# Performance work log

Hardware: AMD Instinct MI355X
Metric: run time of the kernel (lower is better)

## Reference

```python
import jax, jax.numpy as jnp
import numpy as np

B, H_IMG, W_IMG, DIM, HEADS, WS = 8, 56, 56, 768, 12, 14
SEQ = H_IMG * W_IMG
HEAD_DIM = DIM // HEADS
MLP_HID = 4 * DIM
SCALE = HEAD_DIM ** -0.5


def setup_inputs() -> dict:
    key = jax.random.key(0)
    ks = jax.random.split(key, 8)
    s = 0.02
    return {
        "x": jax.random.normal(ks[0], (B, SEQ, DIM), jnp.float32),
        "ln1_scale": jnp.ones((DIM,), jnp.float32),
        "ln1_bias": jnp.zeros((DIM,), jnp.float32),
        "qkv_w": jax.random.normal(ks[1], (DIM, 3 * DIM), jnp.float32) * s,
        "qkv_b": jnp.zeros((3 * DIM,), jnp.float32),
        "rel_pos_h": jax.random.normal(ks[2], (2 * WS - 1, HEAD_DIM), jnp.float32) * s,
        "rel_pos_w": jax.random.normal(ks[3], (2 * WS - 1, HEAD_DIM), jnp.float32) * s,
        "proj_w": jax.random.normal(ks[4], (DIM, DIM), jnp.float32) * s,
        "proj_b": jnp.zeros((DIM,), jnp.float32),
        "ln2_scale": jnp.ones((DIM,), jnp.float32),
        "ln2_bias": jnp.zeros((DIM,), jnp.float32),
        "fc1_w": jax.random.normal(ks[5], (DIM, MLP_HID), jnp.float32) * s,
        "fc1_b": jnp.zeros((MLP_HID,), jnp.float32),
        "fc2_w": jax.random.normal(ks[6], (MLP_HID, DIM), jnp.float32) * s,
        "fc2_b": jnp.zeros((DIM,), jnp.float32),
        "H": H_IMG,
        "W": W_IMG,
    }


def _layernorm(x, scale, bias, eps=1e-5):
    mu = x.mean(-1, keepdims=True)
    var = x.var(-1, keepdims=True)
    return (x - mu) / jnp.sqrt(var + eps) * scale + bias


def _window_attn(x, H, W, qkv_w, qkv_b, rel_pos_h, rel_pos_w, proj_w, proj_b):
    # x: (B, H*W, C); H, W divisible by WS so the torch pad branch is a no-op
    Bn, N, C = x.shape
    nh, nw = H // WS, W // WS
    # window_partition: (B, H, W, C) -> (B*nh*nw, WS*WS, C)
    xw = (x.reshape(Bn, nh, WS, nw, WS, C)
            .transpose(0, 1, 3, 2, 4, 5)
            .reshape(-1, WS * WS, C))
    Bw, Nw = xw.shape[0], WS * WS
    qkv = (xw @ qkv_w + qkv_b).reshape(Bw, Nw, 3, HEADS, HEAD_DIM).transpose(2, 0, 3, 1, 4)
    q = qkv[0] * SCALE  # scaled q also used for rel-pos terms (matches torch)
    k, v = qkv[1], qkv[2]
    attn = jnp.einsum('bhnd,bhmd->bhnm', q, k)  # (Bw, heads, Nw, Nw)
    # relative position bias (q_shape == k_shape == (WS, WS), ratios == 1)
    dist = jnp.arange(WS)[:, None] - jnp.arange(WS)[None, :] + (WS - 1)
    Rh = rel_pos_h[dist]  # (WS, WS, head_dim)
    Rw = rel_pos_w[dist]
    r_q = q.reshape(Bw, HEADS, WS, WS, HEAD_DIM)
    rel_h = jnp.einsum('byhwc,hkc->byhwk', r_q, Rh)
    rel_w = jnp.einsum('byhwc,wkc->byhwk', r_q, Rw)
    attn = (attn.reshape(Bw, HEADS, WS, WS, WS, WS)
            + rel_h[:, :, :, :, :, None]
            + rel_w[:, :, :, :, None, :]).reshape(Bw, HEADS, Nw, Nw)
    attn = jax.nn.softmax(attn, axis=-1)
    out = jnp.einsum('bhnm,bhmd->bhnd', attn, v).transpose(0, 2, 1, 3).reshape(Bw, Nw, C)
    out = out @ proj_w + proj_b
    # window_reverse: (Bw, WS*WS, C) -> (B, H*W, C)
    out = (out.reshape(Bn, nh, nw, WS, WS, C)
              .transpose(0, 1, 3, 2, 4, 5)
              .reshape(Bn, H * W, C))
    return out


def reference(x, ln1_scale, ln1_bias, qkv_w, qkv_b, rel_pos_h, rel_pos_w,
              proj_w, proj_b, ln2_scale, ln2_bias, fc1_w, fc1_b, fc2_w, fc2_b, H, W):
    a = _window_attn(_layernorm(x, ln1_scale, ln1_bias), H, W,
                     qkv_w, qkv_b, rel_pos_h, rel_pos_w, proj_w, proj_b)
    x = x + a
    h = _layernorm(x, ln2_scale, ln2_bias)
    h = jax.nn.gelu(h @ fc1_w + fc1_b, approximate=False)  # torch nn.GELU is exact erf
    x = x + (h @ fc2_w + fc2_b)
    return x
```

## Files before the change

### kernel.cpp

```cpp
#include <hip/hip_runtime.h>
#include <stdint.h>

typedef unsigned short u16;
typedef __bf16 bf16x8 __attribute__((ext_vector_type(8)));
typedef float f32x4 __attribute__((ext_vector_type(4)));
typedef unsigned uint32x4 __attribute__((ext_vector_type(4)));

#define DEVI __device__ __forceinline__

static constexpr int DIM = 768;
static constexpr int SEQL = 3136;
static constexpr int MROWS = 25088;
static constexpr int HEADS = 12;
static constexpr int HD = 64;
static constexpr int NW = 196;
static constexpr float QSCALE = 0.125f;
static constexpr int ATTN_SMEM = 72704;
static constexpr int GEMM_SMEM = 49152;

DEVI float b2f(u16 u) { union { unsigned i; float f; } v; v.i = ((unsigned)u) << 16; return v.f; }
DEVI u16 f2b(float f) { union { float f; unsigned u; } v; v.f = f; return (u16)((v.u + 0x7FFFu + ((v.u >> 16) & 1u)) >> 16); }
DEVI unsigned pack2(float a, float b) { return (unsigned)f2b(a) | ((unsigned)f2b(b) << 16); }
DEVI bf16x8 u4bf(uint4 u) { union { uint4 a; bf16x8 b; } c; c.a = u; return c.b; }

DEVI void gl_lds16(const void* g, void* l) {
  __builtin_amdgcn_global_load_lds((const __attribute__((address_space(1))) void*)g,
                                   (__attribute__((address_space(3))) void*)l, 16, 0, 0);
}

DEVI bf16x8 ldg_b8(const u16* p) {
  union { uint4 u; bf16x8 v; } r;
  const uint2* p2 = (const uint2*)p;
  uint2 lo = p2[0], hi = p2[1];
  r.u.x = lo.x; r.u.y = lo.y; r.u.z = hi.x; r.u.w = hi.y;
  return r.v;
}

__global__ __launch_bounds__(256) void pack_b(const float* __restrict__ in,
                                              u16* __restrict__ out, int K, int N) {
  int f8 = blockIdx.x * 256 + threadIdx.x;
  int l = f8 & 63;
  int rest = f8 >> 6;
  int s = rest & 1, nf = (rest >> 1) & 3, wn2 = (rest >> 3) & 1, kt = rest >> 4;
  int bn = blockIdx.y;
  int n = bn * 128 + wn2 * 64 + nf * 16 + (l & 15);
  int kb = kt * 64 + s * 32 + (l >> 4) * 8;
  size_t obase = (((size_t)bn * (K >> 6) + kt) * 2 + wn2) * 4096 + (nf * 2 + s) * 512 + (size_t)l * 8;
  #pragma unroll
  for (int e = 0; e < 8; ++e)
    out[obase + e] = f2b(in[(size_t)(kb + e) * N + n]);
}

__global__ __launch_bounds__(256) void cvt_rpb(const float* __restrict__ rph,
                                               const float* __restrict__ rpw,
                                               u16* __restrict__ rpb) {
  int i = blockIdx.x * 256 + threadIdx.x;
  int tbl = i >> 11, r = (i >> 6) & 31, c = i & 63;
  float v = (r < 27) ? (tbl ? rpw : rph)[r * 64 + c] : 0.f;
  rpb[i] = f2b(v);
}

template<bool REMAP>
__global__ __launch_bounds__(256) void ln_kernel(const float* __restrict__ xin,
                                                 const float* __restrict__ g,
                                                 const float* __restrict__ bb,
                                                 u16* __restrict__ outw) {
  __shared__ float red[8];
  const int r = blockIdx.x;
  const int tid = threadIdx.x;
  const float* xr = xin + (size_t)r * DIM;
  float v0 = xr[tid], v1 = xr[tid + 256], v2 = xr[tid + 512];
  float s1 = v0 + v1 + v2;
  float s2 = v0 * v0 + v1 * v1 + v2 * v2;
  #pragma unroll
  for (int o = 32; o > 0; o >>= 1) { s1 += __shfl_down(s1, o); s2 += __shfl_down(s2, o); }
  const int l = tid & 63, w = tid >> 6;
  if (l == 0) { red[w] = s1; red[w + 4] = s2; }
  __syncthreads();
  float ts = red[0] + red[1] + red[2] + red[3];
  float tss = red[4] + red[5] + red[6] + red[7];
  float mean = ts * (1.f / 768.f);
  float var = tss * (1.f / 768.f) - mean * mean;
  float rstd = rsqrtf(var + 1e-5f);
  size_t orow;
  if constexpr (REMAP) {
    int b = r / SEQL, s = r % SEQL;
    int h = s / 56, ww = s % 56;
    orow = (size_t)(b * 16 + (h / 14) * 4 + (ww / 14)) * NW + (h % 14) * 14 + (ww % 14);
  } else {
    orow = (size_t)r;
  }
  u16* orp = outw + orow * DIM;
  orp[tid]       = f2b((v0 - mean) * rstd * g[tid]       + bb[tid]);
  orp[tid + 256] = f2b((v1 - mean) * rstd * g[tid + 256] + bb[tid + 256]);
  orp[tid + 512] = f2b((v2 - mean) * rstd * g[tid + 512] + bb[tid + 512]);
}

struct Epi {
  const float* bias;
  const float* x;
  float* outf;
  u16* q; u16* k; u16* v;
  u16* o16;
};

#define MFMA_BF16 __builtin_amdgcn_mfma_f32_16x16x32_bf16

template<int K, int N, int EPI>
__global__ __launch_bounds__(256, 3)
void gemm6_ep(const u16* __restrict__ A, const u16* __restrict__ Bp, Epi ep) {
  extern __shared__ __align__(16) char gsm[];

  constexpr int NBN = N / 128;
  constexpr int NSTC = NBN / 6;
  constexpr int NKT = K / 64;

  const int tid = threadIdx.x;
  const int l = tid & 63, w = tid >> 6;
  const int lr = l & 15, lg = l >> 4;

  const int nwg = gridDim.x;
  const int cpx = nwg >> 3;
  const int wg = (blockIdx.x & 7) * cpx + (blockIdx.x >> 3);
  const int st = wg / 42, r42 = wg - st * 42;
  const int bm = (st / NSTC) * 7 + r42 / 6;
  const int bn = (st - (st / NSTC) * NSTC) * 6 + r42 - (r42 / 6) * 6;
  const int wm = (w >> 1) * 64, wn = (w & 1) * 64;

  const u16* Ab = A + (size_t)bm * 128 * K;
  const u16* Bw = Bp + (((size_t)bn * NKT) * 2 + (w & 1)) * 4096 + (size_t)l * 8;

  int srcoff[4];
  #pragma unroll
  for (int p = 0; p < 4; ++p) {
    int si = p * 256 + tid;
    int row = si >> 3;
    srcoff[p] = row * K + (((si & 7) ^ (row & 7)) << 3);
  }
  #define STG(kt, buf) do {                                                     \
    char* _d = gsm + (buf) * 16384;                                             \
    _Pragma("unroll")                                                           \
    for (int _p = 0; _p < 4; ++_p)                                              \
      gl_lds16(Ab + srcoff[_p] + (size_t)(kt) * 64, _d + _p * 4096 + tid * 16); \
  } while (0)

  const int p0 = lg ^ (lr & 7);
  const int p1 = p0 ^ 4;

  f32x4 zero4 = {0.f, 0.f, 0.f, 0.f};
  f32x4 acc[4][4];
  #pragma unroll
  for (int i = 0; i < 4; ++i)
    #pragma unroll
    for (int j = 0; j < 4; ++j) acc[i][j] = zero4;

  STG(0, 0);
  STG(1, 1);

  for (int t = 0; t < NKT; ++t) {
    if (t + 1 < NKT) asm volatile("s_waitcnt vmcnt(4)" ::: "memory");
    else             asm volatile("s_waitcnt vmcnt(0)" ::: "memory");
    __builtin_amdgcn_s_barrier();

    uint4 braw[4][2];
    const u16* bt = Bw + (size_t)t * 8192;
    #pragma unroll
    for (int nf = 0; nf < 4; ++nf)
      #pragma unroll
      for (int s = 0; s < 2; ++s)
        braw[nf][s] = *(const uint4*)(bt + (nf * 2 + s) * 512);

    if (t + 2 < NKT) STG(t + 2, (t + 2) % 3);

    const u16* cA = (const u16*)(gsm + (t % 3) * 16384);
    bf16x8 af[4][2];
    #pragma unroll
    for (int mf = 0; mf < 4; ++mf) {
      af[mf][0] = *(const bf16x8*)(cA + (wm + mf * 16 + lr) * 64 + p0 * 8);
      af[mf][1] = *(const bf16x8*)(cA + (wm + mf * 16 + lr) * 64 + p1 * 8);
    }
    __builtin_amdgcn_s_setprio(1);
    #pragma unroll
    for (int mf = 0; mf < 4; ++mf)
      #pragma unroll
      for (int nf = 0; nf < 4; ++nf) {
        acc[mf][nf] = MFMA_BF16(af[mf][0], u4bf(braw[nf][0]), acc[mf][nf], 0, 0, 0);
        acc[mf][nf] = MFMA_BF16(af[mf][1], u4bf(braw[nf][1]), acc[mf][nf], 0, 0, 0);
      }
    __builtin_amdgcn_s_setprio(0);
  }
  #undef STG

  __syncthreads();
  float* tp = (float*)(gsm + w * 8448);
  const int ccl = (l & 3) * 16;
  const int cbase = bn * 128 + wn + ccl;
  f32x4 bs[4];
  #pragma unroll
  for (int jj = 0; jj < 4; ++jj) bs[jj] = *(const f32x4*)(ep.bias + cbase + jj * 4);

  #pragma unroll
  for (int q = 0; q < 2; ++q) {
    if (q == 1) { asm volatile("s_waitcnt lgkmcnt(0)" ::: "memory"); __builtin_amdgcn_sched_barrier(0); }
    #pragma unroll
    for (int mf2 = 0; mf2 < 2; ++mf2)
      #pragma unroll
      for (int nf = 0; nf < 4; ++nf)
        #pragma unroll
        for (int e = 0; e < 4; ++e)
          tp[(mf2 * 16 + lg * 4 + e) * 66 + nf * 16 + lr] = acc[q * 2 + mf2][nf][e];
    asm volatile("s_waitcnt lgkmcnt(0)" ::: "memory");
    __builtin_amdgcn_sched_barrier(0);

    #pragma unroll
    for (int pp = 0; pp < 2; ++pp) {
      const int rowl = pp * 16 + (l >> 2);
      const int r = bm * 128 + wm + q * 32 + rowl;
      const int c = cbase;
      f32x4 vv[4];
      #pragma unroll
      for (int jj = 0; jj < 4; ++jj) {
        #pragma unroll
        for (int j2 = 0; j2 < 4; ++j2)
          vv[jj][j2] = tp[rowl * 66 + ccl + jj * 4 + j2];
        vv[jj] += bs[jj];
      }

      if constexpr (EPI == 0) {
        const int which = c / DIM;
        const int hdc = c - which * DIM;
        const int head = hdc >> 6, d0 = hdc & 63;
        const int win = r / NW, pos = r - win * NW;
        const size_t wh = (size_t)win * HEADS + head;
        if (which == 0) {
          uint32x4 o0, o1;
          o0[0] = pack2(vv[0][0] * QSCALE, vv[0][1] * QSCALE);
          o0[1] = pack2(vv[0][2] * QSCALE, vv[0][3] * QSCALE);
          o0[2] = pack2(vv[1][0] * QSCALE, vv[1][1] * QSCALE);
          o0[3] = pack2(vv[1][2] * QSCALE, vv[1][3] * QSCALE);
          o1[0] = pack2(vv[2][0] * QSCALE, vv[2][1] * QSCALE);
          o1[1] = pack2(vv[2][2] * QSCALE, vv[2][3] * QSCALE);
          o1[2] = pack2(vv[3][0] * QSCALE, vv[3][1] * QSCALE);
          o1[3] = pack2(vv[3][2] * QSCALE, vv[3][3] * QSCALE);
          u16* dst = ep.q + (wh * NW + pos) * HD + d0;
          __builtin_nontemporal_store(o0, (uint32x4*)dst);
          __builtin_nontemporal_store(o1, (uint32x4*)(dst + 8));
        } else if (which == 1) {
          uint32x4 o0, o1;
          o0[0] = pack2(vv[0][0], vv[0][1]); o0[1] = pack2(vv[0][2], vv[0][3]);
          o0[2] = pack2(vv[1][0], vv[1][1]); o0[3] = pack2(vv[1][2], vv[1][3]);
          o1[0] = pack2(vv[2][0], vv[2][1]); o1[1] = pack2(vv[2][2], vv[2][3]);
          o1[2] = pack2(vv[3][0], vv[3][1]); o1[3] = pack2(vv[3][2], vv[3][3]);
          u16* dst = ep.k + (wh * NW + pos) * HD + d0;
          __builtin_nontemporal_store(o0, (uint32x4*)dst);
          __builtin_nontemporal_store(o1, (uint32x4*)(dst + 8));
        } else {
          #pragma unroll
          for (int jj = 0; jj < 4; ++jj)
            #pragma unroll
            for (int j2 = 0; j2 < 4; ++j2)
              __builtin_nontemporal_store(f2b(vv[jj][j2]),
                  ep.v + (wh * HD + d0 + jj * 4 + j2) * NW + pos);
        }
      } else if constexpr (EPI == 1) {
        const int win = r / NW, pos = r - win * NW;
        const int b = win >> 4, wi = win & 15;
        const int hh = (wi >> 2) * 14 + pos / 14;
        const int ww2 = (wi & 3) * 14 + pos % 14;
        const size_t orow = (size_t)b * SEQL + hh * 56 + ww2;
        const f32x4* px = (const f32x4*)(ep.x + orow * DIM + c);
        f32x4* po = (f32x4*)(ep.outf + orow * DIM + c);
        #pragma unroll
        for (int jj = 0; jj < 4; ++jj) {
          f32x4 t2 = px[jj] + vv[jj];
          __builtin_nontemporal_store(t2, po + jj);
        }
      } else if constexpr (EPI == 2) {
        float g[16];
        #pragma unroll
        for (int jj = 0; jj < 4; ++jj)
          #pragma unroll
          for (int j2 = 0; j2 < 4; ++j2) {
            float x2 = vv[jj][j2];
            g[jj * 4 + j2] = 0.5f * x2 * (1.f + erff(x2 * 0.70710678118654752f));
          }
        uint32x4 o0, o1;
        o0[0] = pack2(g[0], g[1]);   o0[1] = pack2(g[2], g[3]);
        o0[2] = pack2(g[4], g[5]);   o0[3] = pack2(g[6], g[7]);
        o1[0] = pack2(g[8], g[9]);   o1[1] = pack2(g[10], g[11]);
        o1[2] = pack2(g[12], g[13]); o1[3] = pack2(g[14], g[15]);
        u16* dst = ep.o16 + (size_t)r * N + c;
        __builtin_nontemporal_store(o0, (uint32x4*)dst);
        __builtin_nontemporal_store(o1, (uint32x4*)(dst + 8));
      } else {
        f32x4* po = (f32x4*)(ep.outf + (size_t)r * N + c);
        #pragma unroll
        for (int jj = 0; jj < 4; ++jj) {
          f32x4 t2 = po[jj] + vv[jj];
          __builtin_nontemporal_store(t2, po + jj);
        }
      }
    }
  }
}

__global__ __launch_bounds__(256, 2)
void attn_kernel(const u16* __restrict__ qbuf, const u16* __restrict__ kbuf,
                 const u16* __restrict__ vt, const u16* __restrict__ rpb,
                 u16* __restrict__ abuf) {
  extern __shared__ __align__(16) char smem[];
  u16* sK = (u16*)smem;
  u16* sP = (u16*)(smem + 26624);
  float* sT = (float*)(smem + 56320);

  const int tid = threadIdx.x;
  const int l = tid & 63, w = tid >> 6;
  const int lr = l & 15, lg = l >> 4;
  const int wh = blockIdx.x;
  const int win = wh / HEADS, head = wh - win * HEADS;

  const u16* Qg = qbuf + (size_t)wh * (NW * HD);
  const u16* Kg = kbuf + (size_t)wh * (NW * HD);
  const u16* Vg = vt + (size_t)wh * (HD * NW);

  for (int t = tid; t < 1664; t += 256) {
    int r8 = t >> 3, c8 = t & 7;
    int s = (t & ~7) | (c8 ^ (r8 & 7));
    if (s >= 1568) s &= 1023;
    gl_lds16(Kg + s * 8, (char*)sK + t * 16);
  }
  __syncthreads();

  f32x4 zero4 = {0.f, 0.f, 0.f, 0.f};
  u16* myP = sP + w * (16 * 232);
  float* myT = sT + w * (16 * 64);

  for (int c = 0; c < 4; ++c) {
    const int chunk = w + 4 * c;
    if (chunk > 12) break;

    int qrow = chunk * 16 + lr; if (qrow > 195) qrow = 195;
    bf16x8 aq0 = *(const bf16x8*)(Qg + (size_t)qrow * HD + lg * 8);
    bf16x8 aq1 = *(const bf16x8*)(Qg + (size_t)qrow * HD + 32 + lg * 8);

    f32x4 th[2], tw[2];
    #pragma unroll
    for (int nf2 = 0; nf2 < 2; ++nf2) {
      const u16* bh = rpb + (nf2 * 16 + lr) * 64;
      const u16* bw = rpb + 2048 + (nf2 * 16 + lr) * 64;
      f32x4 a = zero4, b = zero4;
      a = MFMA_BF16(aq0, *(const bf16x8*)(bh + lg * 8), a, 0, 0, 0);
      a = MFMA_BF16(aq1, *(const bf16x8*)(bh + 32 + lg * 8), a, 0, 0, 0);
      b = MFMA_BF16(aq0, *(const bf16x8*)(bw + lg * 8), b, 0, 0, 0);
      b = MFMA_BF16(aq1, *(const bf16x8*)(bw + 32 + lg * 8), b, 0, 0, 0);
      th[nf2] = a; tw[nf2] = b;
    }
    #pragma unroll
    for (int nf2 = 0; nf2 < 2; ++nf2)
      #pragma unroll
      for (int e = 0; e < 4; ++e) {
        myT[(lg * 4 + e) * 64 + nf2 * 16 + lr]      = th[nf2][e];
        myT[(lg * 4 + e) * 64 + 32 + nf2 * 16 + lr] = tw[nf2][e];
      }

    f32x4 accs[13];
    #pragma unroll
    for (int nf = 0; nf < 13; ++nf) {
      int krow = nf * 16 + lr;
      int ksw = (krow & 7) << 3;
      bf16x8 b0 = *(const bf16x8*)(sK + krow * 64 + ((lg * 8) ^ ksw));
      bf16x8 b1 = *(const bf16x8*)(sK + krow * 64 + ((32 + lg * 8) ^ ksw));
      f32x4 cc = zero4;
      cc = MFMA_BF16(aq0, b0, cc, 0, 0, 0);
      cc = MFMA_BF16(aq1, b1, cc, 0, 0, 0);
      accs[nf] = cc;
    }

    int ihv[4], iwv[4];
    #pragma unroll
    for (int e = 0; e < 4; ++e) {
      int gi = chunk * 16 + lg * 4 + e;
      ihv[e] = (gi * 9363) >> 17;
      iwv[e] = gi - ihv[e] * 14;
    }
    float mrow[4] = {-3e38f, -3e38f, -3e38f, -3e38f};
    #pragma unroll
    for (int nf = 0; nf < 13; ++nf) {
      int j = nf * 16 + lr;
      int jh = (j * 9363) >> 17;
      int jw = j - jh * 14;
      #pragma unroll
      for (int e = 0; e < 4; ++e) {
        int ic = lg * 4 + e;
        float s = accs[nf][e]
                + myT[ic * 64 + ((ihv[e] - jh + 13) & 63)]
                + myT[ic * 64 + 32 + (iwv[e] - jw + 13)];
        if (nf == 12 && lr >= 4) s = -1e30f;
        accs[nf][e] = s;
        mrow[e] = fmaxf(mrow[e], s);
      }
    }
    #pragma unroll
    for (int e = 0; e < 4; ++e) {
      float v = mrow[e];
      v = fmaxf(v, __shfl_xor(v, 1)); v = fmaxf(v, __shfl_xor(v, 2));
      v = fmaxf(v, __shfl_xor(v, 4)); v = fmaxf(v, __shfl_xor(v, 8));
      mrow[e] = v;
    }
    float ssum[4] = {0.f, 0.f, 0.f, 0.f};
    #pragma unroll
    for (int nf = 0; nf < 13; ++nf)
      #pragma unroll
      for (int e = 0; e < 4; ++e) {
        float p = __expf(accs[nf][e] - mrow[e]);
        accs[nf][e] = p;
        ssum[e] += p;
      }
    #pragma unroll
    for (int e = 0; e < 4; ++e) {
      float v = ssum[e];
      v += __shfl_xor(v, 1); v += __shfl_xor(v, 2);
      v += __shfl_xor(v, 4); v += __shfl_xor(v, 8);
      ssum[e] = 1.f / v;
    }
    #pragma unroll
    for (int nf = 0; nf < 13; ++nf)
      #pragma unroll
      for (int e = 0; e < 4; ++e)
        myP[(lg * 4 + e) * 232 + nf * 16 + lr] = f2b(accs[nf][e] * ssum[e]);
    #pragma unroll
    for (int e = 0; e < 4; ++e)
      myP[(lg * 4 + e) * 232 + 208 + lr] = 0;

    f32x4 acco[4];
    #pragma unroll
    for (int nf = 0; nf < 4; ++nf) acco[nf] = zero4;
    #pragma unroll
    for (int ks = 0; ks < 7; ++ks) {
      bf16x8 ap = *(const bf16x8*)(myP + lr * 232 + ks * 32 + lg * 8);
      #pragma unroll
      for (int nf = 0; nf < 4; ++nf) {
        bf16x8 bv = ldg_b8(Vg + (size_t)(nf * 16 + lr) * NW + ks * 32 + lg * 8);
        acco[nf] = MFMA_BF16(ap, bv, acco[nf], 0, 0, 0);
      }
    }
    u16* ob = abuf + (size_t)win * NW * DIM + head * HD;
    #pragma unroll
    for (int nf = 0; nf < 4; ++nf)
      #pragma unroll
      for (int e = 0; e < 4; ++e) {
        int row = chunk * 16 + lg * 4 + e;
        if (row < 196) ob[(size_t)row * DIM + nf * 16 + lr] = f2b(acco[nf][e]);
      }
  }
}

extern "C" void kernel_launch(void* const* d_in, const int* in_sizes, int n_in,
                              void* d_out, int out_size, void* d_ws, size_t ws_size,
                              hipStream_t stream) {
  (void)in_sizes; (void)n_in; (void)out_size; (void)ws_size;
  const float* x    = (const float*)d_in[0];
  const float* ln1s = (const float*)d_in[1];
  const float* ln1b = (const float*)d_in[2];
  const float* qkvw = (const float*)d_in[3];
  const float* qkvb = (const float*)d_in[4];
  const float* rph  = (const float*)d_in[5];
  const float* rpw  = (const float*)d_in[6];
  const float* pjw  = (const float*)d_in[7];
  const float* pjb  = (const float*)d_in[8];
  const float* ln2s = (const float*)d_in[9];
  const float* ln2b = (const float*)d_in[10];
  const float* f1w  = (const float*)d_in[11];
  const float* f1b  = (const float*)d_in[12];
  const float* f2w  = (const float*)d_in[13];
  const float* f2b_ = (const float*)d_in[14];
  float* out = (float*)d_out;

  char* ws = (char*)d_ws;
  u16* qkvwT = (u16*)ws;
  u16* projwT = qkvwT + 1769472;
  u16* fc1wT  = qkvwT + 2359296;
  u16* fc2wT  = qkvwT + 4718592;
  u16* xw   = (u16*)(ws + 14155776);
  u16* qbuf = (u16*)(ws + 52690944);
  u16* kbuf = qbuf + 19267584;
  u16* vtb  = kbuf + 19267584;
  u16* h2   = (u16*)(ws + 168296448);
  u16* abuf = xw;
  u16* h1   = xw;
  u16* rpb  = h2;

  (void)hipFuncSetAttribute((const void*)attn_kernel,
                            hipFuncAttributeMaxDynamicSharedMemorySize, ATTN_SMEM);
  (void)hipFuncSetAttribute((const void*)gemm6_ep<768, 2304, 0>,
                            hipFuncAttributeMaxDynamicSharedMemorySize, GEMM_SMEM);
  (void)hipFuncSetAttribute((const void*)gemm6_ep<768, 768, 1>,
                            hipFuncAttributeMaxDynamicSharedMemorySize, GEMM_SMEM);
  (void)hipFuncSetAttribute((const void*)gemm6_ep<768, 3072, 2>,
                            hipFuncAttributeMaxDynamicSharedMemorySize, GEMM_SMEM);
  (void)hipFuncSetAttribute((const void*)gemm6_ep<3072, 768, 3>,
                            hipFuncAttributeMaxDynamicSharedMemorySize, GEMM_SMEM);

  pack_b<<<dim3(768 / 16, 2304 / 128), 256, 0, stream>>>(qkvw, qkvwT, 768, 2304);
  pack_b<<<dim3(768 / 16, 768 / 128),  256, 0, stream>>>(pjw, projwT, 768, 768);
  pack_b<<<dim3(768 / 16, 3072 / 128), 256, 0, stream>>>(f1w, fc1wT, 768, 3072);
  pack_b<<<dim3(3072 / 16, 768 / 128), 256, 0, stream>>>(f2w, fc2wT, 3072, 768);
  cvt_rpb<<<16, 256, 0, stream>>>(rph, rpw, rpb);

  ln_kernel<true><<<MROWS, 256, 0, stream>>>(x, ln1s, ln1b, xw);

  { Epi e{}; e.bias = qkvb; e.q = qbuf; e.k = kbuf; e.v = vtb;
    gemm6_ep<768, 2304, 0><<<196 * 18, 256, GEMM_SMEM, stream>>>(xw, qkvwT, e); }

  attn_kernel<<<1536, 256, ATTN_SMEM, stream>>>(qbuf, kbuf, vtb, rpb, abuf);

  { Epi e{}; e.bias = pjb; e.x = x; e.outf = out;
    gemm6_ep<768, 768, 1><<<196 * 6, 256, GEMM_SMEM, stream>>>(abuf, projwT, e); }

  ln_kernel<false><<<MROWS, 256, 0, stream>>>(out, ln2s, ln2b, h2);

  { Epi e{}; e.bias = f1b; e.o16 = h1;
    gemm6_ep<768, 3072, 2><<<196 * 24, 256, GEMM_SMEM, stream>>>(h2, fc1wT, e); }

  { Epi e{}; e.bias = f2b_; e.outf = out;
    gemm6_ep<3072, 768, 3><<<196 * 6, 256, GEMM_SMEM, stream>>>(h1, fc2wT, e); }
}
```

Measured before the change: 805.8 us.

## Use wave-per-row LayerNorm, coalesced V-transpose stores, and tanh-form GELU

```diff
diff --git a/kernel.cpp b/kernel.cpp
--- a/kernel.cpp
+++ b/kernel.cpp
@@ -5,6 +5,7 @@
 typedef __bf16 bf16x8 __attribute__((ext_vector_type(8)));
 typedef float f32x4 __attribute__((ext_vector_type(4)));
 typedef unsigned uint32x4 __attribute__((ext_vector_type(4)));
+typedef unsigned uint32x2 __attribute__((ext_vector_type(2)));
 
 #define DEVI __device__ __forceinline__
 
@@ -22,6 +23,13 @@
 DEVI u16 f2b(float f) { union { float f; unsigned u; } v; v.f = f; return (u16)((v.u + 0x7FFFu + ((v.u >> 16) & 1u)) >> 16); }
 DEVI unsigned pack2(float a, float b) { return (unsigned)f2b(a) | ((unsigned)f2b(b) << 16); }
 DEVI bf16x8 u4bf(uint4 u) { union { uint4 a; bf16x8 b; } c; c.a = u; return c.b; }
+
+DEVI float gelu_f(float x) {
+  float x2 = x * x;
+  float y = x * (1.5957691216f + 0.0713548162726f * x2);
+  float e = __expf(-y);
+  return x * __builtin_amdgcn_rcpf(1.f + e);
+}
 
 DEVI void gl_lds16(const void* g, void* l) {
   __builtin_amdgcn_global_load_lds((const __attribute__((address_space(1))) void*)g,
@@ -65,22 +73,25 @@
                                                  const float* __restrict__ g,
                                                  const float* __restrict__ bb,
                                                  u16* __restrict__ outw) {
-  __shared__ float red[8];
-  const int r = blockIdx.x;
-  const int tid = threadIdx.x;
+  const int l = threadIdx.x & 63, w = threadIdx.x >> 6;
+  const int r = blockIdx.x * 4 + w;
   const float* xr = xin + (size_t)r * DIM;
-  float v0 = xr[tid], v1 = xr[tid + 256], v2 = xr[tid + 512];
-  float s1 = v0 + v1 + v2;
-  float s2 = v0 * v0 + v1 * v1 + v2 * v2;
-  #pragma unroll
-  for (int o = 32; o > 0; o >>= 1) { s1 += __shfl_down(s1, o); s2 += __shfl_down(s2, o); }
-  const int l = tid & 63, w = tid >> 6;
-  if (l == 0) { red[w] = s1; red[w + 4] = s2; }
-  __syncthreads();
-  float ts = red[0] + red[1] + red[2] + red[3];
-  float tss = red[4] + red[5] + red[6] + red[7];
-  float mean = ts * (1.f / 768.f);
-  float var = tss * (1.f / 768.f) - mean * mean;
+  f32x4 v[3], gv[3], bv[3];
+  #pragma unroll
+  for (int j = 0; j < 3; ++j) {
+    v[j]  = *(const f32x4*)(xr + j * 256 + l * 4);
+    gv[j] = *(const f32x4*)(g  + j * 256 + l * 4);
+    bv[j] = *(const f32x4*)(bb + j * 256 + l * 4);
+  }
+  float s1 = 0.f, s2 = 0.f;
+  #pragma unroll
+  for (int j = 0; j < 3; ++j)
+    #pragma unroll
+    for (int e = 0; e < 4; ++e) { s1 += v[j][e]; s2 += v[j][e] * v[j][e]; }
+  #pragma unroll
+  for (int o = 1; o < 64; o <<= 1) { s1 += __shfl_xor(s1, o); s2 += __shfl_xor(s2, o); }
+  float mean = s1 * (1.f / 768.f);
+  float var = s2 * (1.f / 768.f) - mean * mean;
   float rstd = rsqrtf(var + 1e-5f);
   size_t orow;
   if constexpr (REMAP) {
@@ -91,9 +102,15 @@
     orow = (size_t)r;
   }
   u16* orp = outw + orow * DIM;
-  orp[tid]       = f2b((v0 - mean) * rstd * g[tid]       + bb[tid]);
-  orp[tid + 256] = f2b((v1 - mean) * rstd * g[tid + 256] + bb[tid + 256]);
-  orp[tid + 512] = f2b((v2 - mean) * rstd * g[tid + 512] + bb[tid + 512]);
+  #pragma unroll
+  for (int j = 0; j < 3; ++j) {
+    uint2 o2;
+    o2.x = pack2((v[j][0] - mean) * rstd * gv[j][0] + bv[j][0],
+                 (v[j][1] - mean) * rstd * gv[j][1] + bv[j][1]);
+    o2.y = pack2((v[j][2] - mean) * rstd * gv[j][2] + bv[j][2],
+                 (v[j][3] - mean) * rstd * gv[j][3] + bv[j][3]);
+    *(uint2*)(orp + j * 256 + l * 4) = o2;
+  }
 }
 
 struct Epi {
@@ -195,9 +212,14 @@
   float* tp = (float*)(gsm + w * 8448);
   const int ccl = (l & 3) * 16;
   const int cbase = bn * 128 + wn + ccl;
+  const int col0 = bn * 128 + wn;
   f32x4 bs[4];
   #pragma unroll
   for (int jj = 0; jj < 4; ++jj) bs[jj] = *(const f32x4*)(ep.bias + cbase + jj * 4);
+
+  const bool isV = (EPI == 0) && (col0 >= 2 * DIM);
+  const float bvl = ep.bias[col0 + l];
+  const int vhead = (col0 - 2 * DIM) >> 6;
 
   #pragma unroll
   for (int q = 0; q < 2; ++q) {
@@ -211,6 +233,39 @@
           tp[(mf2 * 16 + lg * 4 + e) * 66 + nf * 16 + lr] = acc[q * 2 + mf2][nf][e];
     asm volatile("s_waitcnt lgkmcnt(0)" ::: "memory");
     __builtin_amdgcn_sched_barrier(0);
+
+    if (isV) {
+      #pragma unroll
+      for (int gidx = 0; gidx < 2; ++gidx) {
+        const int row0 = bm * 128 + wm + q * 32 + gidx * 16;
+        const int win0 = row0 / NW;
+        const int win15 = (row0 + 15) / NW;
+        float vx[16];
+        #pragma unroll
+        for (int i = 0; i < 16; ++i)
+          vx[i] = tp[(gidx * 16 + i) * 66 + l] + bvl;
+        if (win0 == win15) {
+          const int pos0 = row0 - win0 * NW;
+          u16* dst = ep.v + ((size_t)(win0 * HEADS + vhead) * HD + l) * NW + pos0;
+          #pragma unroll
+          for (int jj = 0; jj < 4; ++jj) {
+            uint32x2 o2;
+            o2[0] = pack2(vx[jj * 4 + 0], vx[jj * 4 + 1]);
+            o2[1] = pack2(vx[jj * 4 + 2], vx[jj * 4 + 3]);
+            __builtin_nontemporal_store(o2, (uint32x2*)(dst + jj * 4));
+          }
+        } else {
+          #pragma unroll
+          for (int i = 0; i < 16; ++i) {
+            int row = row0 + i;
+            int win = row / NW, pos = row - win * NW;
+            __builtin_nontemporal_store(f2b(vx[i]),
+                ep.v + ((size_t)(win * HEADS + vhead) * HD + l) * NW + pos);
+          }
+        }
+      }
+      continue;
+    }
 
     #pragma unroll
     for (int pp = 0; pp < 2; ++pp) {
@@ -245,7 +300,7 @@
           u16* dst = ep.q + (wh * NW + pos) * HD + d0;
           __builtin_nontemporal_store(o0, (uint32x4*)dst);
           __builtin_nontemporal_store(o1, (uint32x4*)(dst + 8));
-        } else if (which == 1) {
+        } else {
           uint32x4 o0, o1;
           o0[0] = pack2(vv[0][0], vv[0][1]); o0[1] = pack2(vv[0][2], vv[0][3]);
           o0[2] = pack2(vv[1][0], vv[1][1]); o0[3] = pack2(vv[1][2], vv[1][3]);
@@ -254,13 +309,6 @@
           u16* dst = ep.k + (wh * NW + pos) * HD + d0;
           __builtin_nontemporal_store(o0, (uint32x4*)dst);
           __builtin_nontemporal_store(o1, (uint32x4*)(dst + 8));
-        } else {
-          #pragma unroll
-          for (int jj = 0; jj < 4; ++jj)
-            #pragma unroll
-            for (int j2 = 0; j2 < 4; ++j2)
-              __builtin_nontemporal_store(f2b(vv[jj][j2]),
-                  ep.v + (wh * HD + d0 + jj * 4 + j2) * NW + pos);
         }
       } else if constexpr (EPI == 1) {
         const int win = r / NW, pos = r - win * NW;
@@ -276,19 +324,17 @@
           __builtin_nontemporal_store(t2, po + jj);
         }
       } else if constexpr (EPI == 2) {
-        float g[16];
+        float gg[16];
         #pragma unroll
         for (int jj = 0; jj < 4; ++jj)
           #pragma unroll
-          for (int j2 = 0; j2 < 4; ++j2) {
-            float x2 = vv[jj][j2];
-            g[jj * 4 + j2] = 0.5f * x2 * (1.f + erff(x2 * 0.70710678118654752f));
-          }
+          for (int j2 = 0; j2 < 4; ++j2)
+            gg[jj * 4 + j2] = gelu_f(vv[jj][j2]);
         uint32x4 o0, o1;
-        o0[0] = pack2(g[0], g[1]);   o0[1] = pack2(g[2], g[3]);
-        o0[2] = pack2(g[4], g[5]);   o0[3] = pack2(g[6], g[7]);
-        o1[0] = pack2(g[8], g[9]);   o1[1] = pack2(g[10], g[11]);
-        o1[2] = pack2(g[12], g[13]); o1[3] = pack2(g[14], g[15]);
+        o0[0] = pack2(gg[0], gg[1]);   o0[1] = pack2(gg[2], gg[3]);
+        o0[2] = pack2(gg[4], gg[5]);   o0[3] = pack2(gg[6], gg[7]);
+        o1[0] = pack2(gg[8], gg[9]);   o1[1] = pack2(gg[10], gg[11]);
+        o1[2] = pack2(gg[12], gg[13]); o1[3] = pack2(gg[14], gg[15]);
         u16* dst = ep.o16 + (size_t)r * N + c;
         __builtin_nontemporal_store(o0, (uint32x4*)dst);
         __builtin_nontemporal_store(o1, (uint32x4*)(dst + 8));
@@ -507,7 +553,7 @@
   pack_b<<<dim3(3072 / 16, 768 / 128), 256, 0, stream>>>(f2w, fc2wT, 3072, 768);
   cvt_rpb<<<16, 256, 0, stream>>>(rph, rpw, rpb);
 
-  ln_kernel<true><<<MROWS, 256, 0, stream>>>(x, ln1s, ln1b, xw);
+  ln_kernel<true><<<MROWS / 4, 256, 0, stream>>>(x, ln1s, ln1b, xw);
 
   { Epi e{}; e.bias = qkvb; e.q = qbuf; e.k = kbuf; e.v = vtb;
     gemm6_ep<768, 2304, 0><<<196 * 18, 256, GEMM_SMEM, stream>>>(xw, qkvwT, e); }
@@ -517,7 +563,7 @@
   { Epi e{}; e.bias = pjb; e.x = x; e.outf = out;
     gemm6_ep<768, 768, 1><<<196 * 6, 256, GEMM_SMEM, stream>>>(abuf, projwT, e); }
 
-  ln_kernel<false><<<MROWS, 256, 0, stream>>>(out, ln2s, ln2b, h2);
+  ln_kernel<false><<<MROWS / 4, 256, 0, stream>>>(out, ln2s, ln2b, h2);
 
   { Epi e{}; e.bias = f1b; e.o16 = h1;
     gemm6_ep<768, 3072, 2><<<196 * 24, 256, GEMM_SMEM, stream>>>(h2, fc1wT, e); }
```

Measured after the change: 852.3 us. 1.06x slower.
